# Kernel tuning notes

Hardware: AMD Instinct MI355X
Metric: run time of the kernel (lower is better)

Reference implementation:

```python
import jax, jax.numpy as jnp
import numpy as np


def _attention(v, W, static_hidden, dec_hidden):
    # static_hidden: [B,N,H], dec_hidden: [B,1,H], v: [1,1,H], W: [1,H,2H]
    hidden = jnp.concatenate(
        [static_hidden, jnp.broadcast_to(dec_hidden, static_hidden.shape)], axis=2
    )  # [B,N,2H]
    e = jnp.tanh(jnp.einsum('bnk,hk->bnh', hidden, W[0]))  # W @ hidden^T, done row-wise
    scores = jnp.einsum('bnh,h->bn', e, v[0, 0])  # [B,N]
    return jax.nn.softmax(scores, axis=1)[:, None, :]  # [B,1,N]


def _gru_step(x, h, w_ih, w_hh, b_ih, b_hh):
    # x: [B,H] input, h: [B,H] prev hidden; PyTorch gate order: r | z | n
    gx = x @ w_ih.T + b_ih  # [B,3H]
    gh = h @ w_hh.T + b_hh  # [B,3H]
    H = h.shape[-1]
    r = jax.nn.sigmoid(gx[:, :H] + gh[:, :H])
    z = jax.nn.sigmoid(gx[:, H:2 * H] + gh[:, H:2 * H])
    n = jnp.tanh(gx[:, 2 * H:] + r * gh[:, 2 * H:])
    return (1.0 - z) * n + z * h


def _pointer_scores(v, W, static_hidden, context, state_embedding):
    # energy = cat(static, context, state_emb) -> [B,N,3H]
    energy = jnp.concatenate(
        [static_hidden,
         jnp.broadcast_to(context, static_hidden.shape),
         jnp.broadcast_to(state_embedding, static_hidden.shape)], axis=2)
    e = jnp.tanh(jnp.einsum('bnk,hk->bnh', energy, W[0]))  # [B,N,H]
    return jnp.einsum('bnh,h->bn', e, v[0, 0])  # [B,N]


def setup_inputs() -> dict:
    key = jax.random.key(0)
    B, N, H = 128, 512, 512
    ks = jax.random.split(key, 16)
    s = 0.05
    return {
        'static_hidden': jax.random.normal(ks[0], (B, N, H), jnp.float32),
        'state_embedding': jax.random.normal(ks[1], (B, 1, H), jnp.float32),
        'decoder_hidden': jax.random.normal(ks[2], (B, 1, H), jnp.float32),
        'target_hidden': jax.random.normal(ks[3], (B, 1, H), jnp.float32),
        'last_hh': jax.random.normal(ks[4], (1, B, H), jnp.float32),
        # Pointer params (note: target branch of the original reuses self.v/self.W)
        'ptr_v': jax.random.normal(ks[5], (1, 1, H), jnp.float32) * s,
        'ptr_W': jax.random.normal(ks[6], (1, H, 3 * H), jnp.float32) * s,
        # encoder attention params
        'enc_v': jax.random.normal(ks[7], (1, 1, H), jnp.float32) * s,
        'enc_W': jax.random.normal(ks[8], (1, H, 2 * H), jnp.float32) * s,
        # target attention params
        'tgt_v': jax.random.normal(ks[9], (1, 1, H), jnp.float32) * s,
        'tgt_W': jax.random.normal(ks[10], (1, H, 2 * H), jnp.float32) * s,
        # GRU (single layer) params
        'gru_w_ih': jax.random.normal(ks[11], (3 * H, H), jnp.float32) * s,
        'gru_w_hh': jax.random.normal(ks[12], (3 * H, H), jnp.float32) * s,
        'gru_b_ih': jax.random.normal(ks[13], (3 * H,), jnp.float32) * s,
        'gru_b_hh': jax.random.normal(ks[14], (3 * H,), jnp.float32) * s,
    }


def reference(static_hidden, state_embedding, decoder_hidden, target_hidden, last_hh,
              ptr_v, ptr_W, enc_v, enc_W, tgt_v, tgt_W,
              gru_w_ih, gru_w_hh, gru_b_ih, gru_b_hh):
    # GRU over seq len 1 (batch_first); dropout layers are identity (eval mode)
    h_new = _gru_step(decoder_hidden[:, 0, :], last_hh[0], gru_w_ih, gru_w_hh, gru_b_ih, gru_b_hh)
    rnn_out = h_new[:, None, :]          # [B,1,H]
    new_last_hh = h_new[None]            # [1,B,H]

    # encoder attention + context
    enc_attn = _attention(enc_v, enc_W, static_hidden, rnn_out)   # [B,1,N]
    context = jnp.matmul(enc_attn, static_hidden)                 # [B,1,H]
    probs = _pointer_scores(ptr_v, ptr_W, static_hidden, context, state_embedding)

    # target attention + context (original reuses self.v/self.W for scoring)
    tgt_attn = _attention(tgt_v, tgt_W, static_hidden, target_hidden)
    context_t = jnp.matmul(tgt_attn, static_hidden)
    probs_target = _pointer_scores(ptr_v, ptr_W, static_hidden, context_t, state_embedding)

    probs = 5.0 * probs + probs_target
    return (probs, new_last_hh)
```

## Files before the change

kernel.cpp:

```cpp
#include <hip/hip_runtime.h>
#include <math.h>

#define B 128
#define N 512
#define H 512

typedef __attribute__((ext_vector_type(8))) short short8;
typedef __attribute__((ext_vector_type(4))) float floatx4;

typedef const __attribute__((address_space(1))) unsigned int* gas_t;
typedef __attribute__((address_space(3))) unsigned int* las_t;

__device__ __forceinline__ void gl16(const void* g, void* l){
    __builtin_amdgcn_global_load_lds((gas_t)g, (las_t)l, 16, 0, 0);
}

__device__ __forceinline__ float sigmoidf_(float x){ return 1.0f/(1.0f+__expf(-x)); }

__device__ __forceinline__ float fast_tanh(float x){
    float e = __expf(2.0f*x);
    return 1.0f - __fdividef(2.0f, 1.0f + e);
}

__device__ __forceinline__ unsigned f2bf1(float f){
    unsigned u = __float_as_uint(f);
    u += 0x7FFFu + ((u>>16)&1u);
    return u>>16;
}
__device__ __forceinline__ unsigned pk2(float a, float b){
    return f2bf1(a) | (f2bf1(b)<<16);
}

__global__ __launch_bounds__(256) void k_cast_small(
    const float* __restrict__ encW, const float* __restrict__ tgtW,
    const float* __restrict__ ptrW, const float* __restrict__ wih,
    const float* __restrict__ whh,
    const float* __restrict__ dec, const float* __restrict__ lhh,
    const float* __restrict__ tgt, const float* __restrict__ sem,
    unsigned short* __restrict__ We_s, unsigned short* __restrict__ Wt_s,
    unsigned short* __restrict__ Wp_s, unsigned short* __restrict__ We_d,
    unsigned short* __restrict__ Wt_d, unsigned short* __restrict__ Wp_c,
    unsigned short* __restrict__ Wp_e, unsigned short* __restrict__ Wih_b,
    unsigned short* __restrict__ Whh_b,
    unsigned short* __restrict__ Xbf, unsigned short* __restrict__ Hbf,
    unsigned short* __restrict__ Tbf, unsigned short* __restrict__ Sbf)
{
    int r = blockIdx.x, t = threadIdx.x;
    if (r < 1664){
        int gr = r*4 + (t>>6);
        int col = (t&63)*8;
        const float* src; unsigned short* dst; int pitch, off, row;
        if (gr < 512)      { src=encW; dst=We_s; pitch=2*H; off=0;   row=gr; }
        else if (gr<1024)  { src=tgtW; dst=Wt_s; pitch=2*H; off=0;   row=gr-512; }
        else if (gr<1536)  { src=ptrW; dst=Wp_s; pitch=3*H; off=0;   row=gr-1024; }
        else if (gr<2048)  { src=encW; dst=We_d; pitch=2*H; off=H;   row=gr-1536; }
        else if (gr<2560)  { src=tgtW; dst=Wt_d; pitch=2*H; off=H;   row=gr-2048; }
        else if (gr<3072)  { src=ptrW; dst=Wp_c; pitch=3*H; off=H;   row=gr-2560; }
        else if (gr<3584)  { src=ptrW; dst=Wp_e; pitch=3*H; off=2*H; row=gr-3072; }
        else if (gr<5120)  { src=wih;  dst=Wih_b;pitch=H;   off=0;   row=gr-3584; }
        else               { src=whh;  dst=Whh_b;pitch=H;   off=0;   row=gr-5120; }
        const float* s8 = &src[(size_t)row*pitch + off + col];
        float4 lo = *(const float4*)s8;
        float4 hi = *(const float4*)(s8+4);
        uint4 p;
        p.x = pk2(lo.x,lo.y); p.y = pk2(lo.z,lo.w);
        p.z = pk2(hi.x,hi.y); p.w = pk2(hi.z,hi.w);
        *(uint4*)&dst[(size_t)row*H + col] = p;
    } else {
        int blk = r - 1664; int mat = blk >> 5;
        const float* src = mat==0?dec : mat==1?lhh : mat==2?tgt : sem;
        unsigned short* dst = mat==0?Xbf : mat==1?Hbf : mat==2?Tbf : Sbf;
        size_t i = ((size_t)(blk&31)*256 + t)*8;
        float4 lo = *(const float4*)&src[i];
        float4 hi = *(const float4*)&src[i+4];
        uint4 p;
        p.x = pk2(lo.x,lo.y); p.y = pk2(lo.z,lo.w);
        p.z = pk2(hi.x,hi.y); p.w = pk2(hi.z,hi.w);
        *(uint4*)&dst[i] = p;
    }
}

__device__ __forceinline__ void gemm128_tile(
    const unsigned short* __restrict__ Ab,
    const unsigned short* __restrict__ Bb,
    float* __restrict__ C, int ldc)
{
    __shared__ __align__(16) unsigned short As[128*64];
    __shared__ __align__(16) unsigned short Bs[128*64];
    int t = threadIdx.x;
    int lane = t & 63, wave = t >> 6;
    int wy = wave >> 1, wx = wave & 1;
    int li = lane & 15, quad = lane >> 4;

    floatx4 acc[4][4];
    #pragma unroll
    for (int i=0;i<4;++i)
      #pragma unroll
      for (int j=0;j<4;++j) acc[i][j] = (floatx4)(0.0f);

    for (int kt=0; kt<8; ++kt){
        int k0 = kt*64;
        #pragma unroll
        for (int c=0;c<4;++c){
            int s = c*256 + t;
            int row = s >> 3;
            int kb = (s & 7) ^ (row & 7);
            gl16(&Ab[(size_t)row*512 + k0 + kb*8], &As[(size_t)s*8]);
            gl16(&Bb[(size_t)row*512 + k0 + kb*8], &Bs[(size_t)s*8]);
        }
        __syncthreads();
        #pragma unroll
        for (int ks=0;ks<2;++ks){
            short8 af[4], bg[4];
            #pragma unroll
            for (int i=0;i<4;++i){
                int m = wy*64 + i*16 + li;
                int kb = (ks*4 + quad) ^ (m&7);
                af[i] = *(const short8*)&As[m*64 + kb*8];
            }
            #pragma unroll
            for (int j=0;j<4;++j){
                int h = wx*64 + j*16 + li;
                int kb = (ks*4 + quad) ^ (h&7);
                bg[j] = *(const short8*)&Bs[h*64 + kb*8];
            }
            #pragma unroll
            for (int i=0;i<4;++i)
              #pragma unroll
              for (int j=0;j<4;++j)
                acc[i][j] = __builtin_amdgcn_mfma_f32_16x16x32_bf16(af[i], bg[j], acc[i][j], 0,0,0);
        }
        __syncthreads();
    }
    #pragma unroll
    for (int i=0;i<4;++i)
      #pragma unroll
      for (int j=0;j<4;++j)
        #pragma unroll
        for (int rg=0;rg<4;++rg){
            int m = wy*64 + i*16 + quad*4 + rg;
            int n = wx*64 + j*16 + li;
            C[(size_t)m*ldc + n] = acc[i][j][rg];
        }
}

__device__ __forceinline__ void gemm128_kslice(
    const unsigned short* __restrict__ Ab,
    const unsigned short* __restrict__ Bb,
    float* __restrict__ C, int ldc, int ktbeg, int ktend)
{
    __shared__ __align__(16) unsigned short As[128*64];
    __shared__ __align__(16) unsigned short Bs[128*64];
    int t = threadIdx.x;
    int lane = t & 63, wave = t >> 6;
    int wy = wave >> 1, wx = wave & 1;
    int li = lane & 15, quad = lane >> 4;

    floatx4 acc[4][4];
    #pragma unroll
    for (int i=0;i<4;++i)
      #pragma unroll
      for (int j=0;j<4;++j) acc[i][j] = (floatx4)(0.0f);

    for (int kt=ktbeg; kt<ktend; ++kt){
        int k0 = kt*64;
        #pragma unroll
        for (int c=0;c<4;++c){
            int s = c*256 + t;
            int row = s >> 3;
            int kb = (s & 7) ^ (row & 7);
            gl16(&Ab[(size_t)row*512 + k0 + kb*8], &As[(size_t)s*8]);
            gl16(&Bb[(size_t)row*512 + k0 + kb*8], &Bs[(size_t)s*8]);
        }
        __syncthreads();
        #pragma unroll
        for (int ks=0;ks<2;++ks){
            short8 af[4], bg[4];
            #pragma unroll
            for (int i=0;i<4;++i){
                int m = wy*64 + i*16 + li;
                int kb = (ks*4 + quad) ^ (m&7);
                af[i] = *(const short8*)&As[m*64 + kb*8];
            }
            #pragma unroll
            for (int j=0;j<4;++j){
                int h = wx*64 + j*16 + li;
                int kb = (ks*4 + quad) ^ (h&7);
                bg[j] = *(const short8*)&Bs[h*64 + kb*8];
            }
            #pragma unroll
            for (int i=0;i<4;++i)
              #pragma unroll
              for (int j=0;j<4;++j)
                acc[i][j] = __builtin_amdgcn_mfma_f32_16x16x32_bf16(af[i], bg[j], acc[i][j], 0,0,0);
        }
        __syncthreads();
    }
    #pragma unroll
    for (int i=0;i<4;++i)
      #pragma unroll
      for (int j=0;j<4;++j)
        #pragma unroll
        for (int rg=0;rg<4;++rg){
            int m = wy*64 + i*16 + quad*4 + rg;
            int n = wx*64 + j*16 + li;
            atomicAdd(&C[(size_t)m*ldc + n], acc[i][j][rg]);
        }
}

__device__ __forceinline__ void gemm128_kslice_f32A(
    const float* __restrict__ Af,
    const unsigned short* __restrict__ Bb,
    float* __restrict__ C, int ldc, int ktbeg, int ktend)
{
    __shared__ __align__(16) unsigned short As[128*64];
    __shared__ __align__(16) unsigned short Bs[128*64];
    int t = threadIdx.x;
    int lane = t & 63, wave = t >> 6;
    int wy = wave >> 1, wx = wave & 1;
    int li = lane & 15, quad = lane >> 4;

    floatx4 acc[4][4];
    #pragma unroll
    for (int i=0;i<4;++i)
      #pragma unroll
      for (int j=0;j<4;++j) acc[i][j] = (floatx4)(0.0f);

    for (int kt=ktbeg; kt<ktend; ++kt){
        int k0 = kt*64;
        #pragma unroll
        for (int c=0;c<4;++c){
            int s = c*256 + t;
            int row = s >> 3;
            int kb = (s & 7) ^ (row & 7);
            gl16(&Bb[(size_t)row*512 + k0 + kb*8], &Bs[(size_t)s*8]);
            const float* src = Af + (size_t)row*512 + k0 + kb*8;
            float4 lo = *(const float4*)src;
            float4 hi = *(const float4*)(src+4);
            uint4 p;
            p.x = pk2(lo.x,lo.y); p.y = pk2(lo.z,lo.w);
            p.z = pk2(hi.x,hi.y); p.w = pk2(hi.z,hi.w);
            *(uint4*)&As[(size_t)s*8] = p;
        }
        __syncthreads();
        #pragma unroll
        for (int ks=0;ks<2;++ks){
            short8 af[4], bg[4];
            #pragma unroll
            for (int i=0;i<4;++i){
                int m = wy*64 + i*16 + li;
                int kb = (ks*4 + quad) ^ (m&7);
                af[i] = *(const short8*)&As[m*64 + kb*8];
            }
            #pragma unroll
            for (int j=0;j<4;++j){
                int h = wx*64 + j*16 + li;
                int kb = (ks*4 + quad) ^ (h&7);
                bg[j] = *(const short8*)&Bs[h*64 + kb*8];
            }
            #pragma unroll
            for (int i=0;i<4;++i)
              #pragma unroll
              for (int j=0;j<4;++j)
                acc[i][j] = __builtin_amdgcn_mfma_f32_16x16x32_bf16(af[i], bg[j], acc[i][j], 0,0,0);
        }
        __syncthreads();
    }
    #pragma unroll
    for (int i=0;i<4;++i)
      #pragma unroll
      for (int j=0;j<4;++j)
        #pragma unroll
        for (int rg=0;rg<4;++rg){
            int m = wy*64 + i*16 + quad*4 + rg;
            int n = wx*64 + j*16 + li;
            atomicAdd(&C[(size_t)m*ldc + n], acc[i][j][rg]);
        }
}

__global__ __launch_bounds__(256,2) void k_mega(
    const unsigned short* __restrict__ Xbf, const unsigned short* __restrict__ Hbf,
    const unsigned short* __restrict__ Wih_b, const unsigned short* __restrict__ Whh_b,
    float* __restrict__ gx, float* __restrict__ gh,
    const unsigned short* __restrict__ Tbf, const unsigned short* __restrict__ Sbf,
    const unsigned short* __restrict__ Wt_d, const unsigned short* __restrict__ Wp_e,
    float* __restrict__ d_tgt, float* __restrict__ d_se,
    const float* __restrict__ A, unsigned short* __restrict__ Abf)
{
    int blk = blockIdx.x;
    if (blk < 32){
        const unsigned short *Ab, *Bb; float* C; int ldc;
        if (blk < 24){
            int mat = blk / 12, nt = blk % 12;
            Ab = mat ? Hbf : Xbf;
            Bb = (mat ? Whh_b : Wih_b) + (size_t)nt*128*512;
            C = (mat ? gh : gx) + nt*128;
            ldc = 3*H;
        } else {
            int sub = blk - 24; int mat = sub >> 2, nt = sub & 3;
            Ab = mat==0 ? Tbf : Sbf;
            Bb = (mat==0 ? Wt_d : Wp_e) + (size_t)nt*128*512;
            C = (mat==0 ? d_tgt : d_se) + nt*128;
            ldc = H;
        }
        gemm128_tile(Ab, Bb, C, ldc);
    } else {
        int t = threadIdx.x;
        size_t i = ((size_t)(blk-32)*256 + t)*8;
        float4 lo = *(const float4*)&A[i];
        float4 hi = *(const float4*)&A[i+4];
        uint4 p;
        p.x = pk2(lo.x,lo.y); p.y = pk2(lo.z,lo.w);
        p.z = pk2(hi.x,hi.y); p.w = pk2(hi.z,hi.w);
        *(uint4*)&Abf[i] = p;
    }
}

__global__ __launch_bounds__(256) void k_gru_gate(const float* __restrict__ gx,
    const float* __restrict__ gh, const float* __restrict__ lhh,
    const float* __restrict__ bih, const float* __restrict__ bhh,
    float* __restrict__ out_hh, unsigned short* __restrict__ hnew_bf)
{
    int idx = blockIdx.x*256 + threadIdx.x;
    int b = idx >> 9, k = idx & 511;
    const float* gxb = gx + (size_t)b*(3*H);
    const float* ghb = gh + (size_t)b*(3*H);
    float r = sigmoidf_(gxb[k]     + bih[k]     + ghb[k]     + bhh[k]);
    float z = sigmoidf_(gxb[H+k]   + bih[H+k]   + ghb[H+k]   + bhh[H+k]);
    float n = tanhf(gxb[2*H+k] + bih[2*H+k] + r*(ghb[2*H+k] + bhh[2*H+k]));
    float h = (1.f-z)*n + z*lhh[idx];
    out_hh[idx] = h;
    hnew_bf[idx] = (unsigned short)f2bf1(h);
}

__global__ __launch_bounds__(256,2) void k_bias_enc(
    const unsigned short* __restrict__ HNbf, const unsigned short* __restrict__ We_d,
    float* __restrict__ d_enc)
{
    int nt = blockIdx.x & 3, ks = blockIdx.x >> 2;
    gemm128_kslice(HNbf, We_d + (size_t)nt*128*512, d_enc + nt*128, H, ks*2, ks*2+2);
}

__global__ __launch_bounds__(256,2) void k_dptr_gemm(
    const float* __restrict__ ctx, const float* __restrict__ ctxt,
    const unsigned short* __restrict__ Wp_c,
    float* __restrict__ d_pe, float* __restrict__ d_pt)
{
    int blk = blockIdx.x;
    int mat = blk >> 4, sub = blk & 15;
    int nt = sub & 3, ks = sub >> 2;
    const float* Af = mat ? ctxt : ctx;
    const unsigned short* Bb = Wp_c + (size_t)nt*128*512;
    float* C = (mat ? d_pt : d_pe) + nt*128;
    gemm128_kslice_f32A(Af, Bb, C, H, ks*2, ks*2+2);
}

template<bool BF16A>
__global__ __launch_bounds__(256,2) void k_scores_fused(
    const float* __restrict__ Af, const unsigned short* __restrict__ Abf,
    const unsigned short* __restrict__ We, const unsigned short* __restrict__ Wt,
    const float* __restrict__ d_enc, const float* __restrict__ d_tgt,
    const float* __restrict__ enc_v, const float* __restrict__ tgt_v,
    float* __restrict__ sc_e, float* __restrict__ sc_t)
{
    __shared__ __align__(16) unsigned short As[128*64];
    __shared__ __align__(16) unsigned short Be[128*64];
    __shared__ __align__(16) unsigned short Bt[128*64];
    __shared__ float red_e[2][128], red_t[2][128];
    int blk = blockIdx.x;
    int b = blk >> 2; int nt = blk & 3;
    int n0 = nt*128;
    int t = threadIdx.x;
    int lane = t & 63, wave = t >> 6;
    int wy = wave >> 1, wx = wave & 1;
    int li = lane & 15, quad = lane >> 4;

    float nse[4][4], nst[4][4];
    #pragma unroll
    for (int i=0;i<4;++i)
      #pragma unroll
      for (int rg=0;rg<4;++rg){ nse[i][rg]=0.f; nst[i][rg]=0.f; }

    for (int ht=0; ht<4; ++ht){
        int hb = ht*128;
        floatx4 acc_e[4][4], acc_t[4][4];
        #pragma unroll
        for (int i=0;i<4;++i)
          #pragma unroll
          for (int j=0;j<4;++j){ acc_e[i][j]=(floatx4)(0.0f); acc_t[i][j]=(floatx4)(0.0f); }

        for (int kt=0; kt<8; ++kt){
            int k0 = kt*64;
            #pragma unroll
            for (int c=0;c<4;++c){
                int s = c*256 + t;
                int row = s >> 3;
                int kb = (s & 7) ^ (row & 7);
                if constexpr (BF16A){
                    gl16(&Abf[(size_t)(b*N+n0+row)*H + k0 + kb*8], &As[(size_t)s*8]);
                } else {
                    const float* src = Af + (size_t)(b*N+n0+row)*H + k0 + kb*8;
                    float4 lo = *(const float4*)src;
                    float4 hi = *(const float4*)(src+4);
                    uint4 p;
                    p.x = pk2(lo.x,lo.y); p.y = pk2(lo.z,lo.w);
                    p.z = pk2(hi.x,hi.y); p.w = pk2(hi.z,hi.w);
                    *(uint4*)&As[(size_t)s*8] = p;
                }
                gl16(&We[(size_t)(hb+row)*H + k0 + kb*8], &Be[(size_t)s*8]);
                gl16(&Wt[(size_t)(hb+row)*H + k0 + kb*8], &Bt[(size_t)s*8]);
            }
            __syncthreads();
            #pragma unroll
            for (int ks=0;ks<2;++ks){
                short8 af[4], be[4], bt[4];
                #pragma unroll
                for (int i=0;i<4;++i){
                    int m = wy*64 + i*16 + li;
                    int kb = (ks*4 + quad) ^ (m&7);
                    af[i] = *(const short8*)&As[m*64 + kb*8];
                }
                #pragma unroll
                for (int j=0;j<4;++j){
                    int h = wx*64 + j*16 + li;
                    int kb = (ks*4 + quad) ^ (h&7);
                    be[j] = *(const short8*)&Be[h*64 + kb*8];
                    bt[j] = *(const short8*)&Bt[h*64 + kb*8];
                }
                #pragma unroll
                for (int i=0;i<4;++i)
                  #pragma unroll
                  for (int j=0;j<4;++j){
                    acc_e[i][j] = __builtin_amdgcn_mfma_f32_16x16x32_bf16(af[i], be[j], acc_e[i][j], 0,0,0);
                    acc_t[i][j] = __builtin_amdgcn_mfma_f32_16x16x32_bf16(af[i], bt[j], acc_t[i][j], 0,0,0);
                  }
            }
            __syncthreads();
        }
        #pragma unroll
        for (int j=0;j<4;++j){
            int hm = hb + wx*64 + j*16 + li;
            float dje = d_enc[b*H+hm], vje = enc_v[hm];
            float djt = d_tgt[b*H+hm], vjt = tgt_v[hm];
            #pragma unroll
            for (int i=0;i<4;++i)
              #pragma unroll
              for (int rg=0;rg<4;++rg){
                nse[i][rg] += vje * fast_tanh(acc_e[i][j][rg] + dje);
                nst[i][rg] += vjt * fast_tanh(acc_t[i][j][rg] + djt);
              }
        }
    }
    #pragma unroll
    for (int off=1; off<16; off<<=1)
      #pragma unroll
      for (int i=0;i<4;++i)
        #pragma unroll
        for (int rg=0;rg<4;++rg){
          nse[i][rg] += __shfl_xor(nse[i][rg], off);
          nst[i][rg] += __shfl_xor(nst[i][rg], off);
        }
    if (li==0){
        #pragma unroll
        for (int i=0;i<4;++i)
          #pragma unroll
          for (int rg=0;rg<4;++rg){
            red_e[wx][wy*64 + i*16 + quad*4 + rg] = nse[i][rg];
            red_t[wx][wy*64 + i*16 + quad*4 + rg] = nst[i][rg];
          }
    }
    __syncthreads();
    if (t < 128){
        sc_e[b*N + n0 + t] = red_e[0][t] + red_e[1][t];
    } else {
        int r2 = t - 128;
        sc_t[b*N + n0 + r2] = red_t[0][r2] + red_t[1][r2];
    }
}

template<bool BF16A>
__global__ __launch_bounds__(256) void k_smax_ctx(
    const float* __restrict__ Af, const unsigned short* __restrict__ Abf,
    const float* __restrict__ sc_e, const float* __restrict__ sc_t,
    float* __restrict__ ctx, float* __restrict__ ctxt)
{
    __shared__ float we[512], wt[512];
    __shared__ float buf[256];
    __shared__ float red[4][64][4];
    int b = blockIdx.x >> 2, q = blockIdx.x & 3;
    int t = threadIdx.x;

    {
        float x0 = sc_e[b*N+t], x1 = sc_e[b*N+t+256];
        float m = fmaxf(x0,x1);
        buf[t]=m; __syncthreads();
        for (int s2=128;s2>0;s2>>=1){ if(t<s2) buf[t]=fmaxf(buf[t],buf[t+s2]); __syncthreads(); }
        m = buf[0]; __syncthreads();
        float e0 = __expf(x0-m), e1 = __expf(x1-m);
        buf[t]=e0+e1; __syncthreads();
        for (int s2=128;s2>0;s2>>=1){ if(t<s2) buf[t]+=buf[t+s2]; __syncthreads(); }
        float inv = 1.0f/buf[0]; __syncthreads();
        we[t]=e0*inv; we[t+256]=e1*inv;
    }
    {
        float x0 = sc_t[b*N+t], x1 = sc_t[b*N+t+256];
        float m = fmaxf(x0,x1);
        buf[t]=m; __syncthreads();
        for (int s2=128;s2>0;s2>>=1){ if(t<s2) buf[t]=fmaxf(buf[t],buf[t+s2]); __syncthreads(); }
        m = buf[0]; __syncthreads();
        float e0 = __expf(x0-m), e1 = __expf(x1-m);
        buf[t]=e0+e1; __syncthreads();
        for (int s2=128;s2>0;s2>>=1){ if(t<s2) buf[t]+=buf[t+s2]; __syncthreads(); }
        float inv = 1.0f/buf[0]; __syncthreads();
        wt[t]=e0*inv; wt[t+256]=e1*inv;
    }
    __syncthreads();

    int p = t & 63, nq = t >> 6;
    int cp = q*64 + p;
    float ae0=0.f, ae1=0.f, at0=0.f, at1=0.f;
    if constexpr (BF16A){
        const unsigned* base = (const unsigned*)Abf + (size_t)(b*N + nq*128)*(H/2) + cp;
        for (int n=0;n<128;++n){
            unsigned u = base[(size_t)n*(H/2)];
            float lo = __uint_as_float(u<<16);
            float hi = __uint_as_float(u & 0xFFFF0000u);
            float e = we[nq*128+n], g = wt[nq*128+n];
            ae0 += e*lo; ae1 += e*hi; at0 += g*lo; at1 += g*hi;
        }
    } else {
        const float* base = Af + (size_t)(b*N + nq*128)*H + 2*cp;
        for (int n=0;n<128;++n){
            float2 v = *(const float2*)&base[(size_t)n*H];
            float e = we[nq*128+n], g = wt[nq*128+n];
            ae0 += e*v.x; ae1 += e*v.y; at0 += g*v.x; at1 += g*v.y;
        }
    }
    red[nq][p][0]=ae0; red[nq][p][1]=ae1; red[nq][p][2]=at0; red[nq][p][3]=at1;
    __syncthreads();
    if (t < 64){
        float s0=0.f,s1=0.f,s2=0.f,s3=0.f;
        #pragma unroll
        for (int k2=0;k2<4;++k2){
            s0+=red[k2][t][0]; s1+=red[k2][t][1]; s2+=red[k2][t][2]; s3+=red[k2][t][3];
        }
        int c2 = q*64 + t;
        ctx [(size_t)b*H + 2*c2]   = s0;
        ctx [(size_t)b*H + 2*c2+1] = s1;
        ctxt[(size_t)b*H + 2*c2]   = s2;
        ctxt[(size_t)b*H + 2*c2+1] = s3;
    }
}

template<bool BF16A>
__global__ __launch_bounds__(256,2) void k_probs_mfma(
    const float* __restrict__ Af, const unsigned short* __restrict__ Abf,
    const unsigned short* __restrict__ Wp,
    const float* __restrict__ d_pe, const float* __restrict__ d_pt,
    const float* __restrict__ d_se,
    const float* __restrict__ ptr_v, float* __restrict__ probs)
{
    __shared__ __align__(16) unsigned short As[128*64];
    __shared__ __align__(16) unsigned short Bs[128*64];
    __shared__ float red[2][128];
    int blk = blockIdx.x;
    int b = blk >> 2; int nt = blk & 3;
    int n0 = nt*128;

    int t = threadIdx.x;
    int lane = t & 63, wave = t >> 6;
    int wy = wave >> 1, wx = wave & 1;
    int li = lane & 15, quad = lane >> 4;

    float nsum[4][4];
    #pragma unroll
    for (int i=0;i<4;++i){ nsum[i][0]=0.f;nsum[i][1]=0.f;nsum[i][2]=0.f;nsum[i][3]=0.f; }

    for (int ht=0; ht<4; ++ht){
        int hb = ht*128;
        floatx4 acc[4][4];
        #pragma unroll
        for (int i=0;i<4;++i)
          #pragma unroll
          for (int j=0;j<4;++j) acc[i][j] = (floatx4)(0.0f);

        for (int kt=0; kt<8; ++kt){
            int k0 = kt*64;
            #pragma unroll
            for (int c=0;c<4;++c){
                int s = c*256 + t;
                int row = s >> 3;
                int kb = (s & 7) ^ (row & 7);
                if constexpr (BF16A){
                    gl16(&Abf[(size_t)(b*N+n0+row)*H + k0 + kb*8], &As[(size_t)s*8]);
                } else {
                    const float* src = Af + (size_t)(b*N+n0+row)*H + k0 + kb*8;
                    float4 lo = *(const float4*)src;
                    float4 hi = *(const float4*)(src+4);
                    uint4 p;
                    p.x = pk2(lo.x,lo.y); p.y = pk2(lo.z,lo.w);
                    p.z = pk2(hi.x,hi.y); p.w = pk2(hi.z,hi.w);
                    *(uint4*)&As[(size_t)s*8] = p;
                }
                gl16(&Wp[(size_t)(hb+row)*H + k0 + kb*8], &Bs[(size_t)s*8]);
            }
            __syncthreads();
            #pragma unroll
            for (int ks=0;ks<2;++ks){
                short8 af[4], bg[4];
                #pragma unroll
                for (int i=0;i<4;++i){
                    int m = wy*64 + i*16 + li;
                    int kb = (ks*4 + quad) ^ (m&7);
                    af[i] = *(const short8*)&As[m*64 + kb*8];
                }
                #pragma unroll
                for (int j=0;j<4;++j){
                    int h = wx*64 + j*16 + li;
                    int kb = (ks*4 + quad) ^ (h&7);
                    bg[j] = *(const short8*)&Bs[h*64 + kb*8];
                }
                #pragma unroll
                for (int i=0;i<4;++i)
                  #pragma unroll
                  for (int j=0;j<4;++j)
                    acc[i][j] = __builtin_amdgcn_mfma_f32_16x16x32_bf16(af[i], bg[j], acc[i][j], 0,0,0);
            }
            __syncthreads();
        }
        #pragma unroll
        for (int j=0;j<4;++j){
            int hm = hb + wx*64 + j*16 + li;
            float se = d_se[b*H + hm];
            float de = d_pe[b*H + hm] + se;
            float dt = d_pt[b*H + hm] + se;
            float vj = ptr_v[hm];
            #pragma unroll
            for (int i=0;i<4;++i)
              #pragma unroll
              for (int rg=0;rg<4;++rg){
                float s = acc[i][j][rg];
                nsum[i][rg] += vj * (5.0f*fast_tanh(s + de) + fast_tanh(s + dt));
              }
        }
    }
    #pragma unroll
    for (int off=1; off<16; off<<=1)
      #pragma unroll
      for (int i=0;i<4;++i)
        #pragma unroll
        for (int rg=0;rg<4;++rg)
          nsum[i][rg] += __shfl_xor(nsum[i][rg], off);
    if (li==0){
        #pragma unroll
        for (int i=0;i<4;++i)
          #pragma unroll
          for (int rg=0;rg<4;++rg)
            red[wx][wy*64 + i*16 + quad*4 + rg] = nsum[i][rg];
    }
    __syncthreads();
    if (t < 128)
        probs[b*N + n0 + t] = red[0][t] + red[1][t];
}

extern "C" void kernel_launch(void* const* d_in, const int* in_sizes, int n_in,
                              void* d_out, int out_size, void* d_ws, size_t ws_size,
                              hipStream_t stream)
{
    (void)in_sizes; (void)n_in; (void)out_size;
    const float* A    = (const float*)d_in[0];
    const float* sem  = (const float*)d_in[1];
    const float* dec  = (const float*)d_in[2];
    const float* tgt  = (const float*)d_in[3];
    const float* lhh  = (const float*)d_in[4];
    const float* ptrv = (const float*)d_in[5];
    const float* ptrW = (const float*)d_in[6];
    const float* encv = (const float*)d_in[7];
    const float* encW = (const float*)d_in[8];
    const float* tgtv = (const float*)d_in[9];
    const float* tgtW = (const float*)d_in[10];
    const float* wih  = (const float*)d_in[11];
    const float* whh  = (const float*)d_in[12];
    const float* bih  = (const float*)d_in[13];
    const float* bhh  = (const float*)d_in[14];

    float* probs_out = (float*)d_out;
    float* hh_out    = (float*)d_out + B*N;

    float* ws = (float*)d_ws;
    const size_t S = (size_t)B*H;
    float* d_enc = ws;
    float* d_tgt = ws + S;
    float* d_se  = ws + 2*S;
    float* sc_e  = ws + 3*S;
    float* sc_t  = ws + 4*S;
    float* ctx   = ws + 5*S;
    float* ctxt  = ws + 6*S;
    float* d_pe  = ws + 9*S;
    float* d_pt  = ws + 10*S;
    float* gx    = ws + 11*S;
    float* gh    = ws + 14*S;
    unsigned short* bfb  = (unsigned short*)(ws + 17*S);
    const size_t WH = (size_t)H*H;
    const size_t WG = (size_t)3*H*H;
    unsigned short* We_s  = bfb;
    unsigned short* Wt_s  = We_s + WH;
    unsigned short* Wp_s  = Wt_s + WH;
    unsigned short* We_d  = Wp_s + WH;
    unsigned short* Wt_d  = We_d + WH;
    unsigned short* Wp_c  = Wt_d + WH;
    unsigned short* Wp_e  = Wp_c + WH;
    unsigned short* Wih_b = Wp_e + WH;
    unsigned short* Whh_b = Wih_b + WG;
    unsigned short* Xbf   = Whh_b + WG;
    unsigned short* Hbf   = Xbf + S;
    unsigned short* Tbf   = Hbf + S;
    unsigned short* Sbf   = Tbf + S;
    unsigned short* HNbf  = Sbf + S;
    unsigned short* Abf   = HNbf + S;

    const size_t need_full = 17*S*sizeof(float)
        + (7*WH + 2*WG + 5*S + (size_t)B*N*H) * sizeof(unsigned short);
    const bool big = ws_size >= need_full;

    hipMemsetAsync(d_enc, 0, S*sizeof(float), stream);
    hipMemsetAsync(d_pe, 0, 2*S*sizeof(float), stream);

    k_cast_small<<<1792, 256, 0, stream>>>(encW, tgtW, ptrW, wih, whh,
        dec, lhh, tgt, sem,
        We_s, Wt_s, Wp_s, We_d, Wt_d, Wp_c, Wp_e, Wih_b, Whh_b,
        Xbf, Hbf, Tbf, Sbf);

    int castA_blocks = big ? (int)(((size_t)B*N*H)/(256*8)) : 0;
    k_mega<<<32 + castA_blocks, 256, 0, stream>>>(Xbf, Hbf, Wih_b, Whh_b, gx, gh,
        Tbf, Sbf, Wt_d, Wp_e, d_tgt, d_se, A, Abf);

    k_gru_gate<<<256, 256, 0, stream>>>(gx, gh, lhh, bih, bhh, hh_out, HNbf);

    k_bias_enc<<<16, 256, 0, stream>>>(HNbf, We_d, d_enc);

    if (big)
        k_scores_fused<true ><<<512, 256, 0, stream>>>(A, Abf, We_s, Wt_s, d_enc, d_tgt, encv, tgtv, sc_e, sc_t);
    else
        k_scores_fused<false><<<512, 256, 0, stream>>>(A, Abf, We_s, Wt_s, d_enc, d_tgt, encv, tgtv, sc_e, sc_t);

    if (big)
        k_smax_ctx<true ><<<512, 256, 0, stream>>>(A, Abf, sc_e, sc_t, ctx, ctxt);
    else
        k_smax_ctx<false><<<512, 256, 0, stream>>>(A, Abf, sc_e, sc_t, ctx, ctxt);

    k_dptr_gemm<<<32, 256, 0, stream>>>(ctx, ctxt, Wp_c, d_pe, d_pt);

    if (big)
        k_probs_mfma<true ><<<512, 256, 0, stream>>>(A, Abf, Wp_s, d_pe, d_pt, d_se, ptrv, probs_out);
    else
        k_probs_mfma<false><<<512, 256, 0, stream>>>(A, Abf, Wp_s, d_pe, d_pt, d_se, ptrv, probs_out);
}
```

Baseline: 437.2 us.

## Compute two H-tiles per A-tile load in pointer-score MFMA kernel

The probs kernel now handles the H dimension in two passes of 256 columns instead of four passes of 128, keeping two accumulator sets and two B shared-memory tiles. Each A tile (static_hidden rows) is therefore loaded and converted half as many times, which cuts global traffic and the fp32-to-bf16 conversion cost for A. In exchange it doubles accumulator registers (128 more VGPRs) and adds 16KB of LDS per block, which may cause spills or lower occupancy under launch_bounds(256,2).

```diff
diff --git a/kernel.cpp b/kernel.cpp
--- a/kernel.cpp
+++ b/kernel.cpp
@@ -561,7 +561,8 @@
     const float* __restrict__ ptr_v, float* __restrict__ probs)
 {
     __shared__ __align__(16) unsigned short As[128*64];
-    __shared__ __align__(16) unsigned short Bs[128*64];
+    __shared__ __align__(16) unsigned short B0[128*64];
+    __shared__ __align__(16) unsigned short B1[128*64];
     __shared__ float red[2][128];
     int blk = blockIdx.x;
     int b = blk >> 2; int nt = blk & 3;
@@ -576,13 +577,13 @@
     #pragma unroll
     for (int i=0;i<4;++i){ nsum[i][0]=0.f;nsum[i][1]=0.f;nsum[i][2]=0.f;nsum[i][3]=0.f; }
 
-    for (int ht=0; ht<4; ++ht){
-        int hb = ht*128;
-        floatx4 acc[4][4];
+    for (int hp=0; hp<2; ++hp){
+        int hb0 = hp*256;
+        floatx4 acc0[4][4], acc1[4][4];
         #pragma unroll
         for (int i=0;i<4;++i)
           #pragma unroll
-          for (int j=0;j<4;++j) acc[i][j] = (floatx4)(0.0f);
+          for (int j=0;j<4;++j){ acc0[i][j]=(floatx4)(0.0f); acc1[i][j]=(floatx4)(0.0f); }
 
         for (int kt=0; kt<8; ++kt){
             int k0 = kt*64;
@@ -602,12 +603,13 @@
                     p.z = pk2(hi.x,hi.y); p.w = pk2(hi.z,hi.w);
                     *(uint4*)&As[(size_t)s*8] = p;
                 }
-                gl16(&Wp[(size_t)(hb+row)*H + k0 + kb*8], &Bs[(size_t)s*8]);
+                gl16(&Wp[(size_t)(hb0+row)*H     + k0 + kb*8], &B0[(size_t)s*8]);
+                gl16(&Wp[(size_t)(hb0+128+row)*H + k0 + kb*8], &B1[(size_t)s*8]);
             }
             __syncthreads();
             #pragma unroll
             for (int ks=0;ks<2;++ks){
-                short8 af[4], bg[4];
+                short8 af[4], bg0[4], bg1[4];
                 #pragma unroll
                 for (int i=0;i<4;++i){
                     int m = wy*64 + i*16 + li;
@@ -618,30 +620,36 @@
                 for (int j=0;j<4;++j){
                     int h = wx*64 + j*16 + li;
                     int kb = (ks*4 + quad) ^ (h&7);
-                    bg[j] = *(const short8*)&Bs[h*64 + kb*8];
+                    bg0[j] = *(const short8*)&B0[h*64 + kb*8];
+                    bg1[j] = *(const short8*)&B1[h*64 + kb*8];
                 }
                 #pragma unroll
                 for (int i=0;i<4;++i)
                   #pragma unroll
-                  for (int j=0;j<4;++j)
-                    acc[i][j] = __builtin_amdgcn_mfma_f32_16x16x32_bf16(af[i], bg[j], acc[i][j], 0,0,0);
+                  for (int j=0;j<4;++j){
+                    acc0[i][j] = __builtin_amdgcn_mfma_f32_16x16x32_bf16(af[i], bg0[j], acc0[i][j], 0,0,0);
+                    acc1[i][j] = __builtin_amdgcn_mfma_f32_16x16x32_bf16(af[i], bg1[j], acc1[i][j], 0,0,0);
+                  }
             }
             __syncthreads();
         }
         #pragma unroll
-        for (int j=0;j<4;++j){
-            int hm = hb + wx*64 + j*16 + li;
-            float se = d_se[b*H + hm];
-            float de = d_pe[b*H + hm] + se;
-            float dt = d_pt[b*H + hm] + se;
-            float vj = ptr_v[hm];
-            #pragma unroll
-            for (int i=0;i<4;++i)
-              #pragma unroll
-              for (int rg=0;rg<4;++rg){
-                float s = acc[i][j][rg];
-                nsum[i][rg] += vj * (5.0f*fast_tanh(s + de) + fast_tanh(s + dt));
-              }
+        for (int sub=0; sub<2; ++sub){
+            #pragma unroll
+            for (int j=0;j<4;++j){
+                int hm = hb0 + sub*128 + wx*64 + j*16 + li;
+                float se = d_se[b*H + hm];
+                float de = d_pe[b*H + hm] + se;
+                float dt = d_pt[b*H + hm] + se;
+                float vj = ptr_v[hm];
+                #pragma unroll
+                for (int i=0;i<4;++i)
+                  #pragma unroll
+                  for (int rg=0;rg<4;++rg){
+                    float s = sub ? acc1[i][j][rg] : acc0[i][j][rg];
+                    nsum[i][rg] += vj * (5.0f*fast_tanh(s + de) + fast_tanh(s + dt));
+                  }
+            }
         }
     }
     #pragma unroll
```

Measured after the change: 409.5 us. -6.3%, faster.
